# Kernel optimization log

Measured on AMD Instinct MI355X. Metric: run time of the kernel, lower is better.

## Reference

```python
import jax, jax.numpy as jnp
import numpy as np

B, IDF, CDF, SIZE, H, L = 32, 64, 256, 32, 8, 256
SS = SIZE * SIZE  # size*size = 1024


def setup_inputs() -> dict:
    key = jax.random.key(0)
    k1, k2, k3 = jax.random.split(key, 3)
    return {
        "weightedContext": jax.random.normal(k1, (B, IDF, SS), dtype=jnp.float32),
        "context": jax.random.normal(k2, (B, CDF, L), dtype=jnp.float32),
        # per-head conv1x1 weights: [H, size*size, cdf]
        "W": jax.random.normal(k3, (H, SS, CDF), dtype=jnp.float32) * 0.02,
        "ih": SIZE,
        "iw": SIZE,
    }


def reference(weightedContext, context, W, ih, iw):
    batch, idf = weightedContext.shape[0], weightedContext.shape[1]
    # conv1x1 per head == per-head GEMM over channel dim: [B,H,SS,L]
    sourceC = jnp.einsum("hoc,bcl->bhol", W, context)
    # attention scores: [B,H,idf,L]
    attn = jnp.einsum("bio,bhol->bhil", weightedContext, sourceC)
    # softmax over sourceL (nn.Softmax() on 2D view -> dim=1 == L here)
    attn = jax.nn.softmax(attn, axis=-1)
    # weightedContext_T summed over heads: bmm(sourceC, attn^T) -> [B,idf,SS]
    ctx_out = jnp.einsum("bhol,bhil->bio", sourceC, attn)
    ctx_out = ctx_out.reshape(batch, idf, ih, iw)
    # attnOut: per-head attn transposed [B,L,idf], summed over heads
    attn_out = jnp.sum(attn, axis=1).transpose(0, 2, 1)
    return ctx_out, attn_out
```

## Files before the change

### kernel.cpp

```cpp
#include <hip/hip_runtime.h>
#include <hip/hip_bf16.h>

#define BB 32
#define IDF 64
#define CDF 256
#define SSZ 1024
#define NH 8
#define LL 256
#define KHC 2048

typedef __attribute__((ext_vector_type(8))) _Float16 half8v;
typedef __attribute__((ext_vector_type(4))) float f32x4;

#define GLDS16(g, l) __builtin_amdgcn_global_load_lds(                        \
    (const __attribute__((address_space(1))) void*)(g),                       \
    (__attribute__((address_space(3))) void*)(l), 16, 0, 0)

#define WAIT_ENTER3(NFULL, NHALF)                                             \
  { if (ks < NSTEP - 2)                                                       \
      asm volatile("s_waitcnt vmcnt(" #NFULL ")" ::: "memory");               \
    else if (ks == NSTEP - 2)                                                 \
      asm volatile("s_waitcnt vmcnt(" #NHALF ")" ::: "memory");               \
    else                                                                      \
      asm volatile("s_waitcnt vmcnt(0)" ::: "memory");                        \
    __builtin_amdgcn_s_barrier();                                             \
    __builtin_amdgcn_sched_barrier(0); }
#define BAR_EXIT()                                                            \
  { __builtin_amdgcn_sched_barrier(0);                                        \
    __builtin_amdgcn_s_barrier();                                             \
    __builtin_amdgcn_sched_barrier(0); }
#define LDS_BAR()                                                             \
  { asm volatile("s_waitcnt lgkmcnt(0)" ::: "memory");                        \
    __builtin_amdgcn_s_barrier();                                             \
    __builtin_amdgcn_sched_barrier(0); }

__device__ inline unsigned short f2h(float x) {
  _Float16 h = (_Float16)x;
  return *reinterpret_cast<unsigned short*>(&h);
}
__device__ inline float h2f(unsigned short u) {
  _Float16 h = *reinterpret_cast<_Float16*>(&u);
  return (float)h;
}

__global__ __launch_bounds__(256) void k_prep(const float* __restrict__ wc,
                                              const float* __restrict__ W,
                                              const float* __restrict__ ctx,
                                              unsigned short* __restrict__ wc16,
                                              unsigned short* __restrict__ W16,
                                              unsigned short* __restrict__ ctx16,
                                              unsigned short* __restrict__ Wt16,
                                              unsigned short* __restrict__ cT16) {
  __shared__ float Tt[64][65];
  int blk0 = blockIdx.x;
  int t = threadIdx.x;
  if (blk0 < 6144) {
    int sel = blk0 >> 11;
    int idx = ((blk0 & 2047) * 256 + t) * 4;
    const float* src = (sel == 0) ? wc : (sel == 1) ? W : ctx;
    unsigned short* d = (sel == 0) ? wc16 : (sel == 1) ? W16 : ctx16;
    float4 v = *reinterpret_cast<const float4*>(&src[idx]);
    __align__(8) unsigned short h[4] = {f2h(v.x), f2h(v.y), f2h(v.z), f2h(v.w)};
    *reinterpret_cast<int2*>(&d[idx]) = *reinterpret_cast<int2*>(h);
  } else if (blk0 < 6656) {
    int blk = blk0 - 6144;
    int h = blk >> 6, ot = (blk >> 2) & 15, cq = blk & 3;
    int og = ot * 64, cg = cq * 64;
    int o_l = t >> 4, c4 = (t & 15) * 4;
#pragma unroll
    for (int p = 0; p < 4; ++p) {
      int o = o_l + 16 * p;
      float4 v = *reinterpret_cast<const float4*>(
          &W[((size_t)h * SSZ + og + o) * CDF + cg + c4]);
      Tt[c4 + 0][o] = v.x; Tt[c4 + 1][o] = v.y;
      Tt[c4 + 2][o] = v.z; Tt[c4 + 3][o] = v.w;
    }
    __syncthreads();
    int c_l = t >> 2;
#pragma unroll
    for (int p = 0; p < 4; ++p) {
      int o0 = ((t & 3) + 4 * p) * 4;
      __align__(8) unsigned short hv[4];
#pragma unroll
      for (int j = 0; j < 4; ++j) hv[j] = f2h(Tt[c_l][o0 + j]);
      size_t base = ((size_t)h * CDF + cg + c_l) * SSZ + og + o0;
      *reinterpret_cast<int2*>(&Wt16[base]) = *reinterpret_cast<int2*>(hv);
    }
  } else {
    int blk = blk0 - 6656;
    int b = blk >> 4, cq = (blk >> 2) & 3, lt = blk & 3;
    int cg = cq * 64, lg = lt * 64;
    int c_l = t >> 4, l4 = (t & 15) * 4;
#pragma unroll
    for (int p = 0; p < 4; ++p) {
      int c = c_l + 16 * p;
      float4 v = *reinterpret_cast<const float4*>(
          &ctx[((size_t)b * CDF + cg + c) * LL + lg + l4]);
      Tt[l4 + 0][c] = v.x; Tt[l4 + 1][c] = v.y;
      Tt[l4 + 2][c] = v.z; Tt[l4 + 3][c] = v.w;
    }
    __syncthreads();
    int l_l = t >> 2;
#pragma unroll
    for (int p = 0; p < 4; ++p) {
      int c0 = ((t & 3) + 4 * p) * 4;
      __align__(8) unsigned short hv[4];
#pragma unroll
      for (int j = 0; j < 4; ++j) hv[j] = f2h(Tt[l_l][c0 + j]);
      size_t base = ((size_t)b * LL + lg + l_l) * CDF + cg + c0;
      *reinterpret_cast<int2*>(&cT16[base]) = *reinterpret_cast<int2*>(hv);
    }
  }
}

#define BUFS 16384

__device__ __forceinline__ void st_p1(short* dst,
                                      const short* gA0, const short* gA1,
                                      const short* gB, int wave, int lane, int k0) {
#pragma unroll
  for (int j = 0; j < 3; ++j) {
    int inst = wave * 3 + j;
    if (inst < 4 || inst >= 20) {
      int ai = (inst < 4) ? inst : (inst - 20);
      const short* src = (ai < 2) ? gA0 : gA1;
      int lr = (ai & 1) * 16 + (lane >> 2);
      int gc = (lane & 3) ^ ((lr >> 1) & 3);
      int toff = ((inst < 4) ? 0 : 10240) + ai * 512;
      GLDS16(src + (size_t)lr * SSZ + k0 + gc * 8, dst + toff);
    } else {
      int bi = inst - 4;
      int brow = bi * 16 + (lane >> 2);
      int gc = (lane & 3) ^ ((brow >> 1) & 3);
      GLDS16(gB + (size_t)brow * SSZ + k0 + gc * 8, dst + 2048 + bi * 512);
    }
  }
}
__device__ __forceinline__ void st_p23(short* dst,
                                       const short* gB0, const short* gB1,
                                       int ld, int wave, int lane, int k0) {
#pragma unroll
  for (int j = 0; j < 4; ++j) {
    int inst = wave * 4 + j;
    int g = inst >> 4;
    int r16 = inst & 15;
    int brow = r16 * 16 + (lane >> 2);
    int gc = (lane & 3) ^ ((brow >> 1) & 3);
    const short* src = g ? gB1 : gB0;
    GLDS16(src + (size_t)brow * ld + k0 + gc * 8, dst + g * 8192 + r16 * 512);
  }
}

__global__ __launch_bounds__(512) void k123(const unsigned short* __restrict__ wc16,
                                            const unsigned short* __restrict__ Wt16,
                                            const unsigned short* __restrict__ cT16,
                                            const unsigned short* __restrict__ ctx16,
                                            unsigned short* __restrict__ P16,
                                            unsigned short* __restrict__ N216) {
  __shared__ __align__(16) short S[3 * BUFS + 16384];
  short* P_lds = &S[3 * BUFS];

  int blk = blockIdx.x;
  int h = blk & 7, ih = (blk >> 3) & 1, bp = blk >> 4;
  int ibase = ih * 32;
  int t = threadIdx.x;
  int lane = t & 63, wave = t >> 6;
  int g = wave >> 2, w4 = wave & 3;
  int ln15 = lane & 15, kh = lane >> 4;
  int rowq = (lane >> 4) * 4;

  int b_g = bp * 2 + g;
  int bh_g = b_g * 8 + h;

  const short* gA0 = (const short*)wc16 + (size_t)((bp * 2 + 0) * IDF + ibase) * SSZ;
  const short* gA1 = (const short*)wc16 + (size_t)((bp * 2 + 1) * IDF + ibase) * SSZ;
  const short* gB  = (const short*)Wt16 + (size_t)h * CDF * SSZ;
  const short* gT0 = (const short*)cT16 + (size_t)(bp * 2 + 0) * LL * CDF;
  const short* gT1 = (const short*)cT16 + (size_t)(bp * 2 + 1) * LL * CDF;
  const short* gC0 = (const short*)ctx16 + (size_t)(bp * 2 + 0) * CDF * LL;
  const short* gC1 = (const short*)ctx16 + (size_t)(bp * 2 + 1) * CDF * LL;

  int offA[2], rowM[2], rmask[2];
#pragma unroll
  for (int r = 0; r < 2; ++r) {
    int lr = r * 16 + ln15;
    offA[r] = g * 1024 + lr * 32 + ((kh ^ ((lr >> 1) & 3)) * 8);
    rowM[r] = g * 8192 + lr * 256;
    rmask[r] = lr & 7;
  }
  int offB1[4], offB2[4];
#pragma unroll
  for (int c = 0; c < 4; ++c) {
    int row = w4 * 64 + c * 16 + ln15;
    int swz = ((kh ^ ((row >> 1) & 3)) * 8);
    offB1[c] = 2048 + row * 32 + swz;
    offB2[c] = g * 8192 + row * 32 + swz;
  }

  f32x4 acc[2][4] = {};

  st_p1(&S[0],        gA0, gA1, gB, wave, lane, 0);
  st_p1(&S[BUFS],     gA0, gA1, gB, wave, lane, 32);
  st_p1(&S[2 * BUFS], gA0, gA1, gB, wave, lane, 64);
  int cur = 0;
  {
    const int NSTEP = 32;
#pragma unroll 1
    for (int ks = 0; ks < NSTEP; ++ks) {
      short* Sc = &S[cur * BUFS];
      WAIT_ENTER3(6, 3)
      half8v fa[2], fb[4];
#pragma unroll
      for (int r = 0; r < 2; ++r)
        fa[r] = *reinterpret_cast<const half8v*>(&Sc[offA[r]]);
#pragma unroll
      for (int c = 0; c < 4; ++c)
        fb[c] = *reinterpret_cast<const half8v*>(&Sc[offB1[c]]);
      __builtin_amdgcn_s_setprio(1);
#pragma unroll
      for (int r = 0; r < 2; ++r)
#pragma unroll
        for (int c = 0; c < 4; ++c)
          acc[r][c] = __builtin_amdgcn_mfma_f32_16x16x32_f16(fa[r], fb[c], acc[r][c], 0, 0, 0);
      __builtin_amdgcn_s_setprio(0);
      BAR_EXIT()
      if (ks + 3 < NSTEP)
        st_p1(Sc, gA0, gA1, gB, wave, lane, (ks + 3) * 32);
      cur = (cur == 2) ? 0 : cur + 1;
    }
  }
#pragma unroll
  for (int r = 0; r < 2; ++r)
#pragma unroll
    for (int c = 0; c < 4; ++c)
#pragma unroll
      for (int reg = 0; reg < 4; ++reg) {
        int row = r * 16 + rowq + reg;
        int col = w4 * 64 + c * 16 + ln15;
        P_lds[g * 8192 + row * 256 +
              ((((col >> 3) ^ (row & 7)) << 3) + (col & 7))] =
            (short)f2h(acc[r][c][reg]);
      }
  LDS_BAR()

#pragma unroll
  for (int r = 0; r < 2; ++r)
#pragma unroll
    for (int c = 0; c < 4; ++c) acc[r][c] = (f32x4){0.f, 0.f, 0.f, 0.f};
  st_p23(&S[0],        gT0, gT1, CDF, wave, lane, 0);
  st_p23(&S[BUFS],     gT0, gT1, CDF, wave, lane, 32);
  st_p23(&S[2 * BUFS], gT0, gT1, CDF, wave, lane, 64);
  cur = 0;
  {
    const int NSTEP = 8;
#pragma unroll 1
    for (int ks = 0; ks < NSTEP; ++ks) {
      short* Sc = &S[cur * BUFS];
      WAIT_ENTER3(8, 4)
      half8v fa[2], fb[4];
#pragma unroll
      for (int r = 0; r < 2; ++r) {
        int ck = ((ks * 4 + kh) ^ rmask[r]) << 3;
        fa[r] = *reinterpret_cast<const half8v*>(&P_lds[rowM[r] + ck]);
      }
#pragma unroll
      for (int c = 0; c < 4; ++c)
        fb[c] = *reinterpret_cast<const half8v*>(&Sc[offB2[c]]);
      __builtin_amdgcn_s_setprio(1);
#pragma unroll
      for (int r = 0; r < 2; ++r)
#pragma unroll
        for (int c = 0; c < 4; ++c)
          acc[r][c] = __builtin_amdgcn_mfma_f32_16x16x32_f16(fa[r], fb[c], acc[r][c], 0, 0, 0);
      __builtin_amdgcn_s_setprio(0);
      BAR_EXIT()
      if (ks + 3 < NSTEP)
        st_p23(Sc, gT0, gT1, CDF, wave, lane, (ks + 3) * 32);
      cur = (cur == 2) ? 0 : cur + 1;
    }
  }

  st_p23(&S[0],        gC0, gC1, LL, wave, lane, 0);
  st_p23(&S[BUFS],     gC0, gC1, LL, wave, lane, 32);
  st_p23(&S[2 * BUFS], gC0, gC1, LL, wave, lane, 64);

  float* pm = reinterpret_cast<float*>(&P_lds[g * 8192]);
  float gmax[2][4], ginv[2][4];
#pragma unroll
  for (int r = 0; r < 2; ++r)
#pragma unroll
    for (int reg = 0; reg < 4; ++reg) {
      float m = fmaxf(fmaxf(acc[r][0][reg], acc[r][1][reg]),
                      fmaxf(acc[r][2][reg], acc[r][3][reg]));
#pragma unroll
      for (int msk = 8; msk >= 1; msk >>= 1) m = fmaxf(m, __shfl_xor(m, msk, 64));
      if (ln15 == 0) pm[(r * 16 + rowq + reg) * 4 + w4] = m;
    }
  LDS_BAR()
#pragma unroll
  for (int r = 0; r < 2; ++r)
#pragma unroll
    for (int reg = 0; reg < 4; ++reg) {
      int row = r * 16 + rowq + reg;
      float4 p0 = *reinterpret_cast<const float4*>(&pm[row * 4]);
      gmax[r][reg] = fmaxf(fmaxf(p0.x, p0.y), fmaxf(p0.z, p0.w));
    }
  LDS_BAR()
#pragma unroll
  for (int r = 0; r < 2; ++r)
#pragma unroll
    for (int reg = 0; reg < 4; ++reg) {
      float s = 0.f;
#pragma unroll
      for (int c = 0; c < 4; ++c) {
        acc[r][c][reg] = __expf(acc[r][c][reg] - gmax[r][reg]);
        s += acc[r][c][reg];
      }
#pragma unroll
      for (int msk = 8; msk >= 1; msk >>= 1) s += __shfl_xor(s, msk, 64);
      if (ln15 == 0) pm[(r * 16 + rowq + reg) * 4 + w4] = s;
    }
  LDS_BAR()
#pragma unroll
  for (int r = 0; r < 2; ++r)
#pragma unroll
    for (int reg = 0; reg < 4; ++reg) {
      int row = r * 16 + rowq + reg;
      float4 p0 = *reinterpret_cast<const float4*>(&pm[row * 4]);
      ginv[r][reg] = 1.f / (p0.x + p0.y + p0.z + p0.w);
    }
  LDS_BAR()

  size_t pbase = (size_t)bh_g * IDF * LL + (size_t)ibase * LL;
#pragma unroll
  for (int r = 0; r < 2; ++r)
#pragma unroll
    for (int c = 0; c < 4; ++c)
#pragma unroll
      for (int reg = 0; reg < 4; ++reg) {
        float p = acc[r][c][reg] * ginv[r][reg];
        int row = r * 16 + rowq + reg;
        int col = w4 * 64 + c * 16 + ln15;
        unsigned short ph = f2h(p);
        P16[pbase + (size_t)row * LL + col] = ph;
        P_lds[g * 8192 + row * 256 +
              ((((col >> 3) ^ (row & 7)) << 3) + (col & 7))] = (short)ph;
      }
  LDS_BAR()

#pragma unroll
  for (int r = 0; r < 2; ++r)
#pragma unroll
    for (int c = 0; c < 4; ++c) acc[r][c] = (f32x4){0.f, 0.f, 0.f, 0.f};
  cur = 0;
  {
    const int NSTEP = 8;
#pragma unroll 1
    for (int ks = 0; ks < NSTEP; ++ks) {
      short* Sc = &S[cur * BUFS];
      WAIT_ENTER3(8, 4)
      half8v fa[2], fb[4];
#pragma unroll
      for (int r = 0; r < 2; ++r) {
        int ck = ((ks * 4 + kh) ^ rmask[r]) << 3;
        fa[r] = *reinterpret_cast<const half8v*>(&P_lds[rowM[r] + ck]);
      }
#pragma unroll
      for (int c = 0; c < 4; ++c)
        fb[c] = *reinterpret_cast<const half8v*>(&Sc[offB2[c]]);
      __builtin_amdgcn_s_setprio(1);
#pragma unroll
      for (int r = 0; r < 2; ++r)
#pragma unroll
        for (int c = 0; c < 4; ++c)
          acc[r][c] = __builtin_amdgcn_mfma_f32_16x16x32_f16(fa[r], fb[c], acc[r][c], 0, 0, 0);
      __builtin_amdgcn_s_setprio(0);
      BAR_EXIT()
      if (ks + 3 < NSTEP)
        st_p23(Sc, gC0, gC1, LL, wave, lane, (ks + 3) * 32);
      cur = (cur == 2) ? 0 : cur + 1;
    }
  }

  size_t nbase = (size_t)b_g * IDF * KHC + (size_t)ibase * KHC + h * CDF;
#pragma unroll
  for (int r = 0; r < 2; ++r)
#pragma unroll
    for (int c = 0; c < 4; ++c)
#pragma unroll
      for (int reg = 0; reg < 4; ++reg) {
        int row = r * 16 + rowq + reg;
        int col = w4 * 64 + c * 16 + ln15;
        N216[nbase + (size_t)row * KHC + col] = f2h(acc[r][c][reg]);
      }
}

__device__ __forceinline__ void k4_stage(short* dst,
                                         const short* gA, const short* gB,
                                         int wave, int lane, int kk0, int obase) {
  int h4 = kk0 >> 8, cb = kk0 & 255;
#pragma unroll
  for (int j = 0; j < 3; ++j) {
    int inst = wave * 3 + j;
    if (inst < 4) {
      int rb = inst * 16;
      int r  = rb + (lane >> 2);
      int gc = (lane & 3) ^ ((r >> 1) & 3);
      GLDS16(gA + (size_t)r * KHC + kk0 + gc * 8, dst + rb * 32);
    } else {
      int rb = (inst - 4) * 16;
      int r  = rb + (lane >> 2);
      int gc = (lane & 3) ^ ((r >> 1) & 3);
      GLDS16(gB + (size_t)(h4 * SSZ + obase + r) * CDF + cb + gc * 8,
             dst + 2048 + rb * 32);
    }
  }
}

__global__ __launch_bounds__(256) void k4_mfma(const unsigned short* __restrict__ N216,
                                               const unsigned short* __restrict__ W16,
                                               float* __restrict__ out0,
                                               float* __restrict__ out1) {
  __shared__ __align__(16) short S[3 * 6144];

  int blk = blockIdx.x;
  int g = blk >> 8;
  int r8 = blk & 255;
  int b = r8 >> 3, ot = r8 & 7;
  int obase = ot * 128;
  int t = threadIdx.x;
  int lane = t & 63, wave = t >> 6;
  int ln15 = lane & 15, kh = lane >> 4;

  const short* gA = (const short*)N216 + (size_t)b * IDF * KHC;
  const short* gB = (const short*)W16;

  int offA[4], offB[2];
#pragma unroll
  for (int r = 0; r < 4; ++r) {
    int row = r * 16 + ln15;
    offA[r] = row * 32 + ((kh ^ ((row >> 1) & 3)) * 8);
  }
#pragma unroll
  for (int c = 0; c < 2; ++c) {
    int row = wave * 32 + c * 16 + ln15;
    offB[c] = 2048 + row * 32 + ((kh ^ ((row >> 1) & 3)) * 8);
  }

  int kbase = g * (KHC / 2);
  f32x4 acc[4][2] = {};

  k4_stage(&S[0],        gA, gB, wave, lane, kbase, obase);
  k4_stage(&S[6144],     gA, gB, wave, lane, kbase + 32, obase);
  k4_stage(&S[2 * 6144], gA, gB, wave, lane, kbase + 64, obase);
  int cur = 0;

  const int NSTEP = 32;
#pragma unroll 1
  for (int ks = 0; ks < NSTEP; ++ks) {
    short* Sc = &S[cur * 6144];
    WAIT_ENTER3(6, 3)
    half8v fa[4], fb[2];
#pragma unroll
    for (int r = 0; r < 4; ++r)
      fa[r] = *reinterpret_cast<const half8v*>(&Sc[offA[r]]);
#pragma unroll
    for (int c = 0; c < 2; ++c)
      fb[c] = *reinterpret_cast<const half8v*>(&Sc[offB[c]]);
    __builtin_amdgcn_s_setprio(1);
#pragma unroll
    for (int r = 0; r < 4; ++r)
#pragma unroll
      for (int c = 0; c < 2; ++c)
        acc[r][c] = __builtin_amdgcn_mfma_f32_16x16x32_f16(fa[r], fb[c], acc[r][c], 0, 0, 0);
    __builtin_amdgcn_s_setprio(0);
    BAR_EXIT()
    if (ks + 3 < NSTEP)
      k4_stage(Sc, gA, gB, wave, lane, kbase + (ks + 3) * 32, obase);
    cur = (cur == 2) ? 0 : cur + 1;
  }

  float* dst = (g == 0) ? out0 : out1;
  int rowq = (lane >> 4) * 4;
#pragma unroll
  for (int r = 0; r < 4; ++r)
#pragma unroll
    for (int c = 0; c < 2; ++c)
#pragma unroll
      for (int reg = 0; reg < 4; ++reg)
        dst[((size_t)b * IDF + r * 16 + rowq + reg) * SSZ +
            obase + wave * 32 + c * 16 + ln15] = acc[r][c][reg];
}

__global__ __launch_bounds__(256) void k_epi(const unsigned short* __restrict__ P16,
                                             float* __restrict__ outa,
                                             float* __restrict__ out,
                                             const float* __restrict__ Pbuf) {
  int blk0 = blockIdx.x;
  int tid = threadIdx.x;
  if (blk0 >= 128) {
    int idx = (blk0 - 128) * 256 + tid;
    float4 a = reinterpret_cast<float4*>(out)[idx];
    float4 p = reinterpret_cast<const float4*>(Pbuf)[idx];
    a.x += p.x; a.y += p.y; a.z += p.z; a.w += p.w;
    reinterpret_cast<float4*>(out)[idx] = a;
    return;
  }
  __shared__ float T[64][65];
  int b = blk0 >> 2, lt = blk0 & 3;
  int l0 = lt * 64;
  float4 acc[4];
#pragma unroll
  for (int p = 0; p < 4; ++p) acc[p] = make_float4(0.f, 0.f, 0.f, 0.f);
  for (int h = 0; h < NH; ++h) {
    size_t src = (size_t)(b * NH + h) * IDF * LL;
#pragma unroll
    for (int p = 0; p < 4; ++p) {
      int f = tid + p * 256;
      int i = f >> 4, lc = (f & 15) * 4;
      ushort4 u = *reinterpret_cast<const ushort4*>(&P16[src + i * LL + l0 + lc]);
      acc[p].x += h2f(u.x); acc[p].y += h2f(u.y);
      acc[p].z += h2f(u.z); acc[p].w += h2f(u.w);
    }
  }
#pragma unroll
  for (int p = 0; p < 4; ++p) {
    int f = tid + p * 256;
    int i = f >> 4, lc = (f & 15) * 4;
    T[i][lc + 0] = acc[p].x; T[i][lc + 1] = acc[p].y;
    T[i][lc + 2] = acc[p].z; T[i][lc + 3] = acc[p].w;
  }
  __syncthreads();
#pragma unroll
  for (int p = 0; p < 4; ++p) {
    int f = tid + p * 256;
    int lr = f >> 4, ic = (f & 15) * 4;
    float4 v = {T[ic + 0][lr], T[ic + 1][lr], T[ic + 2][lr], T[ic + 3][lr]};
    *reinterpret_cast<float4*>(&outa[((size_t)b * LL + l0 + lr) * IDF + ic]) = v;
  }
}

extern "C" void kernel_launch(void* const* d_in, const int* in_sizes, int n_in,
                              void* d_out, int out_size, void* d_ws, size_t ws_size,
                              hipStream_t stream) {
  const float* wc  = (const float*)d_in[0];
  const float* ctx = (const float*)d_in[1];
  const float* W   = (const float*)d_in[2];
  float* out = (float*)d_out;

  const size_t NE = 2097152;
  const size_t NM = 4194304;
  unsigned short* p = (unsigned short*)d_ws;
  unsigned short *wc16 = p;   p += NE;
  unsigned short *Wt16 = p;   p += NE;
  unsigned short *W16  = p;   p += NE;
  unsigned short *ctx16 = p;  p += NE;
  unsigned short *cT16 = p;   p += NE;
  unsigned short *P16  = p;   p += NM;
  unsigned short *N216 = p;   p += NM;
  float* Pbuf = (float*)p;

  k_prep  <<<7168, 256, 0, stream>>>(wc, W, ctx, wc16, W16, ctx16, Wt16, cT16);
  k123    <<<256, 512, 0, stream>>>(wc16, Wt16, cT16, ctx16, P16, N216);
  k4_mfma <<<512, 256, 0, stream>>>(N216, W16, out, Pbuf);
  k_epi   <<<2176, 256, 0, stream>>>(P16, out + (size_t)BB * IDF * SSZ, out, Pbuf);
}
```

Before: 78.21 us.

## Swap batch-pairing from k123 to k4: k123 per (b,h) block, k4 pairs batches

k123 now gives each block one batch and one head, covering all 64 idf rows. Before, each block covered a pair of batches and half of the idf rows. This removes the duplicated per-batch loads of context and its transpose in phases two and three and shrinks the staging buffers. k4_mfma moves to 512-thread blocks that process two batches together, so each staged W tile is reused across both batches and the grid is halved. The trade-off is that the weight tile in k123 phase one is now shared by only one batch rather than two. Each wave also issues fewer async loads per stage, so the vmcnt wait thresholds are adjusted to match.

Measured after the change: 76.19 us. 2.6% less time.

```diff
diff --git a/kernel.cpp b/kernel.cpp
--- a/kernel.cpp
+++ b/kernel.cpp
@@ -113,21 +113,19 @@
   }
 }
 
-#define BUFS 16384
-
-__device__ __forceinline__ void st_p1(short* dst,
-                                      const short* gA0, const short* gA1,
-                                      const short* gB, int wave, int lane, int k0) {
+#define BUFS 12288
+
+__device__ __forceinline__ void st_p1(short* dst, const short* gA, const short* gB,
+                                      int wave, int lane, int k0) {
 #pragma unroll
   for (int j = 0; j < 3; ++j) {
     int inst = wave * 3 + j;
     if (inst < 4 || inst >= 20) {
       int ai = (inst < 4) ? inst : (inst - 20);
-      const short* src = (ai < 2) ? gA0 : gA1;
-      int lr = (ai & 1) * 16 + (lane >> 2);
-      int gc = (lane & 3) ^ ((lr >> 1) & 3);
+      int r  = ai * 16 + (lane >> 2);
+      int gc = (lane & 3) ^ ((r >> 1) & 3);
       int toff = ((inst < 4) ? 0 : 10240) + ai * 512;
-      GLDS16(src + (size_t)lr * SSZ + k0 + gc * 8, dst + toff);
+      GLDS16(gA + (size_t)r * SSZ + k0 + gc * 8, dst + toff);
     } else {
       int bi = inst - 4;
       int brow = bi * 16 + (lane >> 2);
@@ -136,18 +134,14 @@
     }
   }
 }
-__device__ __forceinline__ void st_p23(short* dst,
-                                       const short* gB0, const short* gB1,
-                                       int ld, int wave, int lane, int k0) {
-#pragma unroll
-  for (int j = 0; j < 4; ++j) {
-    int inst = wave * 4 + j;
-    int g = inst >> 4;
-    int r16 = inst & 15;
-    int brow = r16 * 16 + (lane >> 2);
+__device__ __forceinline__ void st_p23(short* dst, const short* gB, int ld,
+                                       int wave, int lane, int k0) {
+#pragma unroll
+  for (int j = 0; j < 2; ++j) {
+    int inst = wave * 2 + j;
+    int brow = inst * 16 + (lane >> 2);
     int gc = (lane & 3) ^ ((brow >> 1) & 3);
-    const short* src = g ? gB1 : gB0;
-    GLDS16(src + (size_t)brow * ld + k0 + gc * 8, dst + g * 8192 + r16 * 512);
+    GLDS16(gB + (size_t)brow * ld + k0 + gc * 8, dst + inst * 512);
   }
 }
 
@@ -161,32 +155,26 @@
   short* P_lds = &S[3 * BUFS];
 
   int blk = blockIdx.x;
-  int h = blk & 7, ih = (blk >> 3) & 1, bp = blk >> 4;
-  int ibase = ih * 32;
+  int b = blk >> 3, h = blk & 7;
   int t = threadIdx.x;
   int lane = t & 63, wave = t >> 6;
   int g = wave >> 2, w4 = wave & 3;
   int ln15 = lane & 15, kh = lane >> 4;
   int rowq = (lane >> 4) * 4;
 
-  int b_g = bp * 2 + g;
-  int bh_g = b_g * 8 + h;
-
-  const short* gA0 = (const short*)wc16 + (size_t)((bp * 2 + 0) * IDF + ibase) * SSZ;
-  const short* gA1 = (const short*)wc16 + (size_t)((bp * 2 + 1) * IDF + ibase) * SSZ;
-  const short* gB  = (const short*)Wt16 + (size_t)h * CDF * SSZ;
-  const short* gT0 = (const short*)cT16 + (size_t)(bp * 2 + 0) * LL * CDF;
-  const short* gT1 = (const short*)cT16 + (size_t)(bp * 2 + 1) * LL * CDF;
-  const short* gC0 = (const short*)ctx16 + (size_t)(bp * 2 + 0) * CDF * LL;
-  const short* gC1 = (const short*)ctx16 + (size_t)(bp * 2 + 1) * CDF * LL;
-
-  int offA[2], rowM[2], rmask[2];
+  const short* gA = (const short*)wc16 + (size_t)b * IDF * SSZ;
+  const short* gB = (const short*)Wt16 + (size_t)h * CDF * SSZ;
+  const short* gT = (const short*)cT16 + (size_t)b * LL * CDF;
+  const short* gC = (const short*)ctx16 + (size_t)b * CDF * LL;
+
+  int offA[2], rowM[2], rmask[2], grow[2];
 #pragma unroll
   for (int r = 0; r < 2; ++r) {
-    int lr = r * 16 + ln15;
-    offA[r] = g * 1024 + lr * 32 + ((kh ^ ((lr >> 1) & 3)) * 8);
-    rowM[r] = g * 8192 + lr * 256;
-    rmask[r] = lr & 7;
+    int row = g * 32 + r * 16 + ln15;
+    grow[r] = row;
+    offA[r] = row * 32 + ((kh ^ ((row >> 1) & 3)) * 8);
+    rowM[r] = row * 256;
+    rmask[r] = row & 7;
   }
   int offB1[4], offB2[4];
 #pragma unroll
@@ -194,14 +182,14 @@
     int row = w4 * 64 + c * 16 + ln15;
     int swz = ((kh ^ ((row >> 1) & 3)) * 8);
     offB1[c] = 2048 + row * 32 + swz;
-    offB2[c] = g * 8192 + row * 32 + swz;
+    offB2[c] = row * 32 + swz;
   }
 
   f32x4 acc[2][4] = {};
 
-  st_p1(&S[0],        gA0, gA1, gB, wave, lane, 0);
-  st_p1(&S[BUFS],     gA0, gA1, gB, wave, lane, 32);
-  st_p1(&S[2 * BUFS], gA0, gA1, gB, wave, lane, 64);
+  st_p1(&S[0],        gA, gB, wave, lane, 0);
+  st_p1(&S[BUFS],     gA, gB, wave, lane, 32);
+  st_p1(&S[2 * BUFS], gA, gB, wave, lane, 64);
   int cur = 0;
   {
     const int NSTEP = 32;
@@ -225,7 +213,7 @@
       __builtin_amdgcn_s_setprio(0);
       BAR_EXIT()
       if (ks + 3 < NSTEP)
-        st_p1(Sc, gA0, gA1, gB, wave, lane, (ks + 3) * 32);
+        st_p1(Sc, gA, gB, wave, lane, (ks + 3) * 32);
       cur = (cur == 2) ? 0 : cur + 1;
     }
   }
@@ -235,10 +223,9 @@
     for (int c = 0; c < 4; ++c)
 #pragma unroll
       for (int reg = 0; reg < 4; ++reg) {
-        int row = r * 16 + rowq + reg;
+        int row = g * 32 + r * 16 + rowq + reg;
         int col = w4 * 64 + c * 16 + ln15;
-        P_lds[g * 8192 + row * 256 +
-              ((((col >> 3) ^ (row & 7)) << 3) + (col & 7))] =
+        P_lds[row * 256 + ((((col >> 3) ^ (row & 7)) << 3) + (col & 7))] =
             (short)f2h(acc[r][c][reg]);
       }
   LDS_BAR()
@@ -247,16 +234,16 @@
   for (int r = 0; r < 2; ++r)
 #pragma unroll
     for (int c = 0; c < 4; ++c) acc[r][c] = (f32x4){0.f, 0.f, 0.f, 0.f};
-  st_p23(&S[0],        gT0, gT1, CDF, wave, lane, 0);
-  st_p23(&S[BUFS],     gT0, gT1, CDF, wave, lane, 32);
-  st_p23(&S[2 * BUFS], gT0, gT1, CDF, wave, lane, 64);
+  st_p23(&S[0],        gT, CDF, wave, lane, 0);
+  st_p23(&S[BUFS],     gT, CDF, wave, lane, 32);
+  st_p23(&S[2 * BUFS], gT, CDF, wave, lane, 64);
   cur = 0;
   {
     const int NSTEP = 8;
 #pragma unroll 1
     for (int ks = 0; ks < NSTEP; ++ks) {
       short* Sc = &S[cur * BUFS];
-      WAIT_ENTER3(8, 4)
+      WAIT_ENTER3(4, 2)
       half8v fa[2], fb[4];
 #pragma unroll
       for (int r = 0; r < 2; ++r) {
@@ -275,16 +262,16 @@
       __builtin_amdgcn_s_setprio(0);
       BAR_EXIT()
       if (ks + 3 < NSTEP)
-        st_p23(Sc, gT0, gT1, CDF, wave, lane, (ks + 3) * 32);
+        st_p23(Sc, gT, CDF, wave, lane, (ks + 3) * 32);
       cur = (cur == 2) ? 0 : cur + 1;
     }
   }
 
-  st_p23(&S[0],        gC0, gC1, LL, wave, lane, 0);
-  st_p23(&S[BUFS],     gC0, gC1, LL, wave, lane, 32);
-  st_p23(&S[2 * BUFS], gC0, gC1, LL, wave, lane, 64);
-
-  float* pm = reinterpret_cast<float*>(&P_lds[g * 8192]);
+  st_p23(&S[0],        gC, LL, wave, lane, 0);
+  st_p23(&S[BUFS],     gC, LL, wave, lane, 32);
+  st_p23(&S[2 * BUFS], gC, LL, wave, lane, 64);
+
+  float* pm = reinterpret_cast<float*>(P_lds);
   float gmax[2][4], ginv[2][4];
 #pragma unroll
   for (int r = 0; r < 2; ++r)
@@ -294,14 +281,14 @@
                       fmaxf(acc[r][2][reg], acc[r][3][reg]));
 #pragma unroll
       for (int msk = 8; msk >= 1; msk >>= 1) m = fmaxf(m, __shfl_xor(m, msk, 64));
-      if (ln15 == 0) pm[(r * 16 + rowq + reg) * 4 + w4] = m;
+      if (ln15 == 0) pm[(g * 32 + r * 16 + rowq + reg) * 4 + w4] = m;
     }
   LDS_BAR()
 #pragma unroll
   for (int r = 0; r < 2; ++r)
 #pragma unroll
     for (int reg = 0; reg < 4; ++reg) {
-      int row = r * 16 + rowq + reg;
+      int row = g * 32 + r * 16 + rowq + reg;
       float4 p0 = *reinterpret_cast<const float4*>(&pm[row * 4]);
       gmax[r][reg] = fmaxf(fmaxf(p0.x, p0.y), fmaxf(p0.z, p0.w));
     }
@@ -318,20 +305,20 @@
       }
 #pragma unroll
       for (int msk = 8; msk >= 1; msk >>= 1) s += __shfl_xor(s, msk, 64);
-      if (ln15 == 0) pm[(r * 16 + rowq + reg) * 4 + w4] = s;
+      if (ln15 == 0) pm[(g * 32 + r * 16 + rowq + reg) * 4 + w4] = s;
     }
   LDS_BAR()
 #pragma unroll
   for (int r = 0; r < 2; ++r)
 #pragma unroll
     for (int reg = 0; reg < 4; ++reg) {
-      int row = r * 16 + rowq + reg;
+      int row = g * 32 + r * 16 + rowq + reg;
       float4 p0 = *reinterpret_cast<const float4*>(&pm[row * 4]);
       ginv[r][reg] = 1.f / (p0.x + p0.y + p0.z + p0.w);
     }
   LDS_BAR()
 
-  size_t pbase = (size_t)bh_g * IDF * LL + (size_t)ibase * LL;
+  size_t pbase = (size_t)blk * IDF * LL;
 #pragma unroll
   for (int r = 0; r < 2; ++r)
 #pragma unroll
@@ -339,12 +326,11 @@
 #pragma unroll
       for (int reg = 0; reg < 4; ++reg) {
         float p = acc[r][c][reg] * ginv[r][reg];
-        int row = r * 16 + rowq + reg;
+        int row = g * 32 + r * 16 + rowq + reg;
         int col = w4 * 64 + c * 16 + ln15;
         unsigned short ph = f2h(p);
         P16[pbase + (size_t)row * LL + col] = ph;
-        P_lds[g * 8192 + row * 256 +
-              ((((col >> 3) ^ (row & 7)) << 3) + (col & 7))] = (short)ph;
+        P_lds[row * 256 + ((((col >> 3) ^ (row & 7)) << 3) + (col & 7))] = (short)ph;
       }
   LDS_BAR()
 
@@ -358,7 +344,7 @@
 #pragma unroll 1
     for (int ks = 0; ks < NSTEP; ++ks) {
       short* Sc = &S[cur * BUFS];
-      WAIT_ENTER3(8, 4)
+      WAIT_ENTER3(4, 2)
       half8v fa[2], fb[4];
 #pragma unroll
       for (int r = 0; r < 2; ++r) {
@@ -377,89 +363,95 @@
       __builtin_amdgcn_s_setprio(0);
       BAR_EXIT()
       if (ks + 3 < NSTEP)
-        st_p23(Sc, gC0, gC1, LL, wave, lane, (ks + 3) * 32);
+        st_p23(Sc, gC, LL, wave, lane, (ks + 3) * 32);
       cur = (cur == 2) ? 0 : cur + 1;
     }
   }
 
-  size_t nbase = (size_t)b_g * IDF * KHC + (size_t)ibase * KHC + h * CDF;
+  size_t nbase = (size_t)b * IDF * KHC + h * CDF;
 #pragma unroll
   for (int r = 0; r < 2; ++r)
 #pragma unroll
     for (int c = 0; c < 4; ++c)
 #pragma unroll
       for (int reg = 0; reg < 4; ++reg) {
-        int row = r * 16 + rowq + reg;
+        int row = g * 32 + r * 16 + rowq + reg;
         int col = w4 * 64 + c * 16 + ln15;
         N216[nbase + (size_t)row * KHC + col] = f2h(acc[r][c][reg]);
       }
 }
 
 __device__ __forceinline__ void k4_stage(short* dst,
-                                         const short* gA, const short* gB,
+                                         const short* gA0, const short* gA1,
+                                         const short* gW,
                                          int wave, int lane, int kk0, int obase) {
   int h4 = kk0 >> 8, cb = kk0 & 255;
 #pragma unroll
-  for (int j = 0; j < 3; ++j) {
-    int inst = wave * 3 + j;
-    if (inst < 4) {
-      int rb = inst * 16;
+  for (int j = 0; j < 2; ++j) {
+    int inst = wave * 2 + j;
+    if (inst < 8) {
+      int gi = inst >> 2;
+      int rb = (inst & 3) * 16;
       int r  = rb + (lane >> 2);
       int gc = (lane & 3) ^ ((r >> 1) & 3);
-      GLDS16(gA + (size_t)r * KHC + kk0 + gc * 8, dst + rb * 32);
+      const short* src = gi ? gA1 : gA0;
+      GLDS16(src + (size_t)r * KHC + kk0 + gc * 8, dst + gi * 2048 + rb * 32);
     } else {
-      int rb = (inst - 4) * 16;
-      int r  = rb + (lane >> 2);
-      int gc = (lane & 3) ^ ((r >> 1) & 3);
-      GLDS16(gB + (size_t)(h4 * SSZ + obase + r) * CDF + cb + gc * 8,
-             dst + 2048 + rb * 32);
-    }
-  }
-}
-
-__global__ __launch_bounds__(256) void k4_mfma(const unsigned short* __restrict__ N216,
+      int bi = inst - 8;
+      int brow = bi * 16 + (lane >> 2);
+      int gc = (lane & 3) ^ ((brow >> 1) & 3);
+      GLDS16(gW + (size_t)(h4 * SSZ + obase + brow) * CDF + cb + gc * 8,
+             dst + 4096 + bi * 512);
+    }
+  }
+}
+
+__global__ __launch_bounds__(512) void k4_mfma(const unsigned short* __restrict__ N216,
                                                const unsigned short* __restrict__ W16,
                                                float* __restrict__ out0,
                                                float* __restrict__ out1) {
-  __shared__ __align__(16) short S[3 * 6144];
+  __shared__ __align__(16) short S[3 * 8192];
 
   int blk = blockIdx.x;
-  int g = blk >> 8;
-  int r8 = blk & 255;
-  int b = r8 >> 3, ot = r8 & 7;
+  int g = blk >> 7;
+  int r7 = blk & 127;
+  int bp = r7 >> 3, ot = r7 & 7;
   int obase = ot * 128;
   int t = threadIdx.x;
   int lane = t & 63, wave = t >> 6;
+  int gr = wave >> 2, w4 = wave & 3;
   int ln15 = lane & 15, kh = lane >> 4;
 
-  const short* gA = (const short*)N216 + (size_t)b * IDF * KHC;
-  const short* gB = (const short*)W16;
+  int b = bp * 2 + gr;
+  const short* gA0 = (const short*)N216 + (size_t)(bp * 2 + 0) * IDF * KHC;
+  const short* gA1 = (const short*)N216 + (size_t)(bp * 2 + 1) * IDF * KHC;
+  const short* gW  = (const short*)W16;
 
   int offA[4], offB[2];
 #pragma unroll
   for (int r = 0; r < 4; ++r) {
     int row = r * 16 + ln15;
-    offA[r] = row * 32 + ((kh ^ ((row >> 1) & 3)) * 8);
+    offA[r] = gr * 2048 + row * 32 + ((kh ^ ((row >> 1) & 3)) * 8);
   }
 #pragma unroll
   for (int c = 0; c < 2; ++c) {
-    int row = wave * 32 + c * 16 + ln15;
-    offB[c] = 2048 + row * 32 + ((kh ^ ((row >> 1) & 3)) * 8);
+    int row = w4 * 32 + c * 16 + ln15;
+    offB[c] = 4096 + row * 32 + ((kh ^ ((row >> 1) & 3)) * 8);
   }
 
   int kbase = g * (KHC / 2);
   f32x4 acc[4][2] = {};
 
-  k4_stage(&S[0],        gA, gB, wave, lane, kbase, obase);
-  k4_stage(&S[6144],     gA, gB, wave, lane, kbase + 32, obase);
-  k4_stage(&S[2 * 6144], gA, gB, wave, lane, kbase + 64, obase);
+  k4_stage(&S[0],        gA0, gA1, gW, wave, lane, kbase, obase);
+  k4_stage(&S[8192],     gA0, gA1, gW, wave, lane, kbase + 32, obase);
+  k4_stage(&S[2 * 8192], gA0, gA1, gW, wave, lane, kbase + 64, obase);
   int cur = 0;
 
   const int NSTEP = 32;
 #pragma unroll 1
   for (int ks = 0; ks < NSTEP; ++ks) {
-    short* Sc = &S[cur * 6144];
-    WAIT_ENTER3(6, 3)
+    short* Sc = &S[cur * 8192];
+    WAIT_ENTER3(4, 2)
     half8v fa[4], fb[2];
 #pragma unroll
     for (int r = 0; r < 4; ++r)
@@ -476,7 +468,7 @@
     __builtin_amdgcn_s_setprio(0);
     BAR_EXIT()
     if (ks + 3 < NSTEP)
-      k4_stage(Sc, gA, gB, wave, lane, kbase + (ks + 3) * 32, obase);
+      k4_stage(Sc, gA0, gA1, gW, wave, lane, kbase + (ks + 3) * 32, obase);
     cur = (cur == 2) ? 0 : cur + 1;
   }
 
@@ -489,7 +481,7 @@
 #pragma unroll
       for (int reg = 0; reg < 4; ++reg)
         dst[((size_t)b * IDF + r * 16 + rowq + reg) * SSZ +
-            obase + wave * 32 + c * 16 + ln15] = acc[r][c][reg];
+            obase + w4 * 32 + c * 16 + ln15] = acc[r][c][reg];
 }
 
 __global__ __launch_bounds__(256) void k_epi(const unsigned short* __restrict__ P16,
@@ -562,6 +554,6 @@
 
   k_prep  <<<7168, 256, 0, stream>>>(wc, W, ctx, wc16, W16, ctx16, Wt16, cT16);
   k123    <<<256, 512, 0, stream>>>(wc16, Wt16, cT16, ctx16, P16, N216);
-  k4_mfma <<<512, 256, 0, stream>>>(N216, W16, out, Pbuf);
+  k4_mfma <<<256, 512, 0, stream>>>(N216, W16, out, Pbuf);
   k_epi   <<<2176, 256, 0, stream>>>(P16, out + (size_t)BB * IDF * SSZ, out, Pbuf);
 }
```
